# Optimization experiments

Measured on AMD Instinct MI355X. Metric: run time of the kernel, lower is better.

The kernel has to match this reference:

```python
import jax, jax.numpy as jnp
import numpy as np


def _lstm_selu(x, W, U, b):
    """Keras-semantics LSTM with activation='selu', return_sequences=True.
    x: [B, T, F]; W: [F, 4H]; U: [H, 4H]; b: [4H]. Gate order i, f, g, o.
    """
    B = x.shape[0]
    H = U.shape[0]
    # Precompute the input projection for all timesteps (one big GEMM).
    xz = jnp.einsum('btf,fg->btg', x, W) + b  # [B, T, 4H]

    def step(carry, xt):
        h, c = carry
        z = xt + h @ U  # [B, 4H]
        i, f, g, o = jnp.split(z, 4, axis=-1)
        i = jax.nn.sigmoid(i)
        f = jax.nn.sigmoid(f)
        g = jax.nn.selu(g)          # activation='selu' on candidate
        o = jax.nn.sigmoid(o)
        c = f * c + i * g
        h = o * jax.nn.selu(c)      # activation='selu' on cell output
        return (h, c), h

    h0 = jnp.zeros((B, H), x.dtype)
    c0 = jnp.zeros((B, H), x.dtype)
    (_, _), hs = jax.lax.scan(step, (h0, c0), jnp.swapaxes(xz, 0, 1))  # hs: [T, B, H]
    return jnp.swapaxes(hs, 0, 1)  # [B, T, H]


def setup_inputs() -> dict:
    key = jax.random.key(0)
    ks = jax.random.split(key, 6)
    B, T, F, H = 64, 2048, 64, 128
    s_in1 = 1.0 / np.sqrt(F)
    s_rec = 1.0 / np.sqrt(H)
    return {
        'x': jax.random.normal(ks[0], (B, T, F), dtype=jnp.float32),
        'W1': jax.random.normal(ks[1], (F, 4 * H), dtype=jnp.float32) * s_in1,
        'U1': jax.random.normal(ks[2], (H, 4 * H), dtype=jnp.float32) * s_rec,
        'b1': jnp.zeros((4 * H,), dtype=jnp.float32),
        'W2': jax.random.normal(ks[3], (H, 4 * H), dtype=jnp.float32) * s_rec,
        'U2': jax.random.normal(ks[4], (H, 4 * H), dtype=jnp.float32) * s_rec,
        'b2': jnp.zeros((4 * H,), dtype=jnp.float32),
    }


def reference(x, W1, U1, b1, W2, U2, b2):
    h1 = _lstm_selu(x, W1, U1, b1)   # layer 1, return_sequences=True
    h2 = _lstm_selu(h1, W2, U2, b2)  # layer 2 consumes layer-1 sequence
    return h2
```

## Files before the change

kernel.cpp:

```cpp
#include <hip/hip_runtime.h>
#include <hip/hip_bf16.h>

#define BATCH 64
#define SEQT  2048
#define FEAT  64
#define HID   128
#define G4    512
#define CHUNK 16
#define NCHUNK (SEQT / CHUNK)
#define XSP  68
#define H1P  136
#define XZP  516

using short8  = __attribute__((ext_vector_type(8))) short;
using floatx4 = __attribute__((ext_vector_type(4))) float;

#define BAR_LGKM() asm volatile("s_waitcnt lgkmcnt(0)\n\ts_barrier" ::: "memory")

__device__ __forceinline__ float sigmoidf_(float x) {
    return __builtin_amdgcn_rcpf(1.0f + __expf(-x));
}
__device__ __forceinline__ float seluf_(float x) {
    const float a = 1.6732632423543772f;
    const float s = 1.0507009873554805f;
    return x > 0.0f ? s * x : s * a * (__expf(x) - 1.0f);
}
__device__ __forceinline__ unsigned short f2bf_(float f) {
    unsigned u = __float_as_uint(f);
    u += 0x7FFFu + ((u >> 16) & 1u);
    return (unsigned short)(u >> 16);
}

__global__ __launch_bounds__(512)
__attribute__((amdgpu_waves_per_eu(2, 2)))
void fused_lstm(const float* __restrict__ x,
                const float* __restrict__ W1,
                const float* __restrict__ U1,
                const float* __restrict__ b1,
                const float* __restrict__ W2,
                const float* __restrict__ U2,
                const float* __restrict__ b2,
                unsigned long long* __restrict__ h1g,
                unsigned* __restrict__ flags,
                float* __restrict__ out) {
    const bool l2  = blockIdx.x >= BATCH;
    const int  b   = l2 ? ((int)blockIdx.x - BATCH) : (int)blockIdx.x;
    const int tid  = threadIdx.x;
    const int w    = tid >> 6;
    const int lane = tid & 63;
    const int c16  = lane & 15;
    const int quad = lane >> 4;
    const int j    = w * 16 + c16;

    __shared__ __align__(16) short hA[2][HID];
    __shared__ __align__(16) float xzbuf[CHUNK * XZP];
    __shared__ __align__(16) float xs[CHUNK * XSP];
    __shared__ __align__(16) short h1c[CHUNK * H1P];
    __shared__ __align__(16) short h1buf[CHUNK * HID];
    __shared__ __align__(16) float hbuf[CHUNK * HID];

    const float* U = l2 ? U2 : U1;
    short8 bfrag[4][4];
#pragma unroll
    for (int g = 0; g < 4; ++g) {
        const float* Ucol = U + (size_t)(g * 128 + j);
#pragma unroll
        for (int kc = 0; kc < 4; ++kc) {
            short8 v;
#pragma unroll
            for (int jj = 0; jj < 8; ++jj) {
                int k = kc * 32 + quad * 8 + jj;
                v[jj] = (short)f2bf_(Ucol[(size_t)k * G4]);
            }
            bfrag[g][kc] = v;
        }
    }

    const float* Wp = l2 ? W2 : W1;
    const int KCW = l2 ? 4 : 2;
    short8 wfrag[4][4];
#pragma unroll
    for (int g = 0; g < 4; ++g) {
        const float* Wcol = Wp + (size_t)(g * 128 + j);
#pragma unroll
        for (int kc = 0; kc < 4; ++kc) {
            if (kc < KCW) {
                short8 v;
#pragma unroll
                for (int jj = 0; jj < 8; ++jj) {
                    int k = kc * 32 + quad * 8 + jj;
                    v[jj] = (short)f2bf_(Wcol[(size_t)k * G4]);
                }
                wfrag[g][kc] = v;
            }
        }
    }
    const float* bb = l2 ? b2 : b1;
    const float4 bias4 = make_float4(bb[j], bb[128 + j], bb[256 + j], bb[384 + j]);

    const float* xb = x + (size_t)b * SEQT * FEAT;
    if (!l2) {
        if (tid < 256) {
            float4 v = ((const float4*)xb)[tid];
            *(float4*)&xs[(tid >> 4) * XSP + ((tid & 15) << 2)] = v;
        }
    }
    if (tid < HID) hA[0][tid] = 0;
    float cst = 0.0f;
    floatx4 zero4 = {0.f, 0.f, 0.f, 0.f};
    __syncthreads();

    float*              out_b = out + (size_t)b * SEQT * HID;
    unsigned long long* h1g_b = h1g + (size_t)b * (SEQT * HID / 4);

    for (int c = 0; c < NCHUNK; ++c) {
        float4 pf;
        if (!l2) {
            if (c + 1 < NCHUNK && tid < 256)
                pf = ((const float4*)(xb + (size_t)(c + 1) * CHUNK * FEAT))[tid];
            short8 ax[2];
#pragma unroll
            for (int kc = 0; kc < 2; ++kc) {
                const float* p = &xs[c16 * XSP + kc * 32 + quad * 8];
                float4 f0 = *(const float4*)p;
                float4 f1 = *(const float4*)(p + 4);
                short8 v;
                v[0] = (short)f2bf_(f0.x); v[1] = (short)f2bf_(f0.y);
                v[2] = (short)f2bf_(f0.z); v[3] = (short)f2bf_(f0.w);
                v[4] = (short)f2bf_(f1.x); v[5] = (short)f2bf_(f1.y);
                v[6] = (short)f2bf_(f1.z); v[7] = (short)f2bf_(f1.w);
                ax[kc] = v;
            }
            floatx4 acc1[4];
#pragma unroll
            for (int g = 0; g < 4; ++g) {
                floatx4 t = __builtin_amdgcn_mfma_f32_16x16x32_bf16(ax[0], wfrag[g][0], zero4, 0, 0, 0);
                acc1[g] = __builtin_amdgcn_mfma_f32_16x16x32_bf16(ax[1], wfrag[g][1], t, 0, 0, 0);
            }
#pragma unroll
            for (int r = 0; r < 4; ++r) {
                int srow = quad * 4 + r;
                *(float4*)&xzbuf[srow * XZP + j * 4] =
                    make_float4(acc1[0][r] + bias4.x, acc1[1][r] + bias4.y,
                                acc1[2][r] + bias4.z, acc1[3][r] + bias4.w);
            }
            __syncthreads();
        } else {
            if (tid == 0) {
                while (__hip_atomic_load(&flags[b], __ATOMIC_RELAXED,
                                         __HIP_MEMORY_SCOPE_AGENT) < (unsigned)(c + 1))
                    __builtin_amdgcn_s_sleep(2);
            }
            __syncthreads();
            {
                unsigned long long hv = __hip_atomic_load(
                    h1g_b + (size_t)c * 512 + tid, __ATOMIC_RELAXED, __HIP_MEMORY_SCOPE_AGENT);
                int t = tid >> 5, kg = tid & 31;
                *(unsigned long long*)&h1c[t * H1P + kg * 4] = hv;
            }
            __syncthreads();

            short8 ah[4];
#pragma unroll
            for (int kc = 0; kc < 4; ++kc)
                ah[kc] = *(const short8*)&h1c[c16 * H1P + kc * 32 + quad * 8];
            floatx4 acc2[4];
#pragma unroll
            for (int g = 0; g < 4; ++g) {
                floatx4 t = __builtin_amdgcn_mfma_f32_16x16x32_bf16(ah[0], wfrag[g][0], zero4, 0, 0, 0);
                t = __builtin_amdgcn_mfma_f32_16x16x32_bf16(ah[1], wfrag[g][1], t, 0, 0, 0);
                t = __builtin_amdgcn_mfma_f32_16x16x32_bf16(ah[2], wfrag[g][2], t, 0, 0, 0);
                acc2[g] = __builtin_amdgcn_mfma_f32_16x16x32_bf16(ah[3], wfrag[g][3], t, 0, 0, 0);
            }
#pragma unroll
            for (int r = 0; r < 4; ++r) {
                int srow = quad * 4 + r;
                *(float4*)&xzbuf[srow * XZP + j * 4] =
                    make_float4(acc2[0][r] + bias4.x, acc2[1][r] + bias4.y,
                                acc2[2][r] + bias4.z, acc2[3][r] + bias4.w);
            }
            __syncthreads();
        }

#pragma unroll 2
        for (int s = 0; s < CHUNK; ++s) {
            float4 xq = *(const float4*)&xzbuf[s * XZP + j * 4];
            const short* hb = &hA[s & 1][0];
            short8 af[4];
#pragma unroll
            for (int kc = 0; kc < 4; ++kc)
                af[kc] = *(const short8*)&hb[kc * 32 + quad * 8];

            floatx4 accA[4], accB[4];
#pragma unroll
            for (int g = 0; g < 4; ++g) {
                floatx4 t0 = __builtin_amdgcn_mfma_f32_16x16x32_bf16(af[0], bfrag[g][0], zero4, 0, 0, 0);
                accA[g] = __builtin_amdgcn_mfma_f32_16x16x32_bf16(af[1], bfrag[g][1], t0, 0, 0, 0);
                floatx4 t1 = __builtin_amdgcn_mfma_f32_16x16x32_bf16(af[2], bfrag[g][2], zero4, 0, 0, 0);
                accB[g] = __builtin_amdgcn_mfma_f32_16x16x32_bf16(af[3], bfrag[g][3], t1, 0, 0, 0);
            }

            float zi = accA[0][0] + accB[0][0] + xq.x;
            float zf = accA[1][0] + accB[1][0] + xq.y;
            float zg = accA[2][0] + accB[2][0] + xq.z;
            float zo = accA[3][0] + accB[3][0] + xq.w;
            float ig = sigmoidf_(zi), fg = sigmoidf_(zf);
            float gg = seluf_(zg),   og = sigmoidf_(zo);
            cst = fg * cst + ig * gg;
            float h = og * seluf_(cst);

            if (lane < 16) {
                unsigned short h16 = f2bf_(h);
                hA[(s + 1) & 1][j] = (short)h16;
                if (l2) hbuf[s * HID + j] = h;
                else    h1buf[s * HID + j] = (short)h16;
            }
            BAR_LGKM();
        }

        if (!l2) {
            unsigned long long hv = *(const unsigned long long*)&h1buf[tid * 4];
            __hip_atomic_store(h1g_b + (size_t)c * 512 + tid, hv,
                               __ATOMIC_RELAXED, __HIP_MEMORY_SCOPE_AGENT);
            if (c + 1 < NCHUNK && tid < 256)
                *(float4*)&xs[(tid >> 4) * XSP + ((tid & 15) << 2)] = pf;
            __syncthreads();
            if (tid == 0)
                __hip_atomic_store(&flags[b], (unsigned)(c + 1),
                                   __ATOMIC_RELAXED, __HIP_MEMORY_SCOPE_AGENT);
        } else {
            float4 hv = *(const float4*)&hbuf[tid * 4];
            *(float4*)&out_b[(size_t)c * CHUNK * HID + tid * 4] = hv;
        }
    }
}

extern "C" void kernel_launch(void* const* d_in, const int* in_sizes, int n_in,
                              void* d_out, int out_size, void* d_ws, size_t ws_size,
                              hipStream_t stream) {
    const float* x  = (const float*)d_in[0];
    const float* W1 = (const float*)d_in[1];
    const float* U1 = (const float*)d_in[2];
    const float* b1 = (const float*)d_in[3];
    const float* W2 = (const float*)d_in[4];
    const float* U2 = (const float*)d_in[5];
    const float* b2 = (const float*)d_in[6];
    float* out = (float*)d_out;

    const size_t BT       = (size_t)BATCH * SEQT;
    const size_t H1_BYTES = BT * HID * 2;

    unsigned long long* h1g   = (unsigned long long*)d_ws;
    unsigned*           flags = (unsigned*)((char*)d_ws + H1_BYTES);

    hipMemsetAsync(flags, 0, BATCH * sizeof(unsigned), stream);

    fused_lstm<<<dim3(2 * BATCH), dim3(512), 0, stream>>>(
        x, W1, U1, b1, W2, U2, b2, h1g, flags, out);
}
```

Before: 1.287 ms.

## Double chunk size to 32 and write layer-2 outputs directly to global

Raises the timestep chunk from 16 to 32, so the input-projection MFMAs, the flag polling, the cross-layer handoff and their block barriers run half as often, each covering two 16-row M tiles. Layer 2 now stores each h value straight to global memory inside the step loop rather than staging a chunk in shared memory and copying it out. The larger chunk increases the lag before layer 2 can start and raises shared-memory use. The per-step scattered global stores add traffic to the latency-critical recurrent loop.

```diff
diff --git a/kernel.cpp b/kernel.cpp
--- a/kernel.cpp
+++ b/kernel.cpp
@@ -6,7 +6,7 @@
 #define FEAT  64
 #define HID   128
 #define G4    512
-#define CHUNK 16
+#define CHUNK 32
 #define NCHUNK (SEQT / CHUNK)
 #define XSP  68
 #define H1P  136
@@ -57,7 +57,6 @@
     __shared__ __align__(16) float xs[CHUNK * XSP];
     __shared__ __align__(16) short h1c[CHUNK * H1P];
     __shared__ __align__(16) short h1buf[CHUNK * HID];
-    __shared__ __align__(16) float hbuf[CHUNK * HID];
 
     const float* U = l2 ? U2 : U1;
     short8 bfrag[4][4];
@@ -100,10 +99,8 @@
 
     const float* xb = x + (size_t)b * SEQT * FEAT;
     if (!l2) {
-        if (tid < 256) {
-            float4 v = ((const float4*)xb)[tid];
-            *(float4*)&xs[(tid >> 4) * XSP + ((tid & 15) << 2)] = v;
-        }
+        float4 v = ((const float4*)xb)[tid];
+        *(float4*)&xs[(tid >> 4) * XSP + ((tid & 15) << 2)] = v;
     }
     if (tid < HID) hA[0][tid] = 0;
     float cst = 0.0f;
@@ -116,33 +113,36 @@
     for (int c = 0; c < NCHUNK; ++c) {
         float4 pf;
         if (!l2) {
-            if (c + 1 < NCHUNK && tid < 256)
+            if (c + 1 < NCHUNK)
                 pf = ((const float4*)(xb + (size_t)(c + 1) * CHUNK * FEAT))[tid];
-            short8 ax[2];
-#pragma unroll
-            for (int kc = 0; kc < 2; ++kc) {
-                const float* p = &xs[c16 * XSP + kc * 32 + quad * 8];
-                float4 f0 = *(const float4*)p;
-                float4 f1 = *(const float4*)(p + 4);
-                short8 v;
-                v[0] = (short)f2bf_(f0.x); v[1] = (short)f2bf_(f0.y);
-                v[2] = (short)f2bf_(f0.z); v[3] = (short)f2bf_(f0.w);
-                v[4] = (short)f2bf_(f1.x); v[5] = (short)f2bf_(f1.y);
-                v[6] = (short)f2bf_(f1.z); v[7] = (short)f2bf_(f1.w);
-                ax[kc] = v;
-            }
-            floatx4 acc1[4];
-#pragma unroll
-            for (int g = 0; g < 4; ++g) {
-                floatx4 t = __builtin_amdgcn_mfma_f32_16x16x32_bf16(ax[0], wfrag[g][0], zero4, 0, 0, 0);
-                acc1[g] = __builtin_amdgcn_mfma_f32_16x16x32_bf16(ax[1], wfrag[g][1], t, 0, 0, 0);
-            }
-#pragma unroll
-            for (int r = 0; r < 4; ++r) {
-                int srow = quad * 4 + r;
-                *(float4*)&xzbuf[srow * XZP + j * 4] =
-                    make_float4(acc1[0][r] + bias4.x, acc1[1][r] + bias4.y,
-                                acc1[2][r] + bias4.z, acc1[3][r] + bias4.w);
+#pragma unroll
+            for (int mt = 0; mt < 2; ++mt) {
+                short8 ax[2];
+#pragma unroll
+                for (int kc = 0; kc < 2; ++kc) {
+                    const float* p = &xs[(mt * 16 + c16) * XSP + kc * 32 + quad * 8];
+                    float4 f0 = *(const float4*)p;
+                    float4 f1 = *(const float4*)(p + 4);
+                    short8 v;
+                    v[0] = (short)f2bf_(f0.x); v[1] = (short)f2bf_(f0.y);
+                    v[2] = (short)f2bf_(f0.z); v[3] = (short)f2bf_(f0.w);
+                    v[4] = (short)f2bf_(f1.x); v[5] = (short)f2bf_(f1.y);
+                    v[6] = (short)f2bf_(f1.z); v[7] = (short)f2bf_(f1.w);
+                    ax[kc] = v;
+                }
+                floatx4 acc1[4];
+#pragma unroll
+                for (int g = 0; g < 4; ++g) {
+                    floatx4 t = __builtin_amdgcn_mfma_f32_16x16x32_bf16(ax[0], wfrag[g][0], zero4, 0, 0, 0);
+                    acc1[g] = __builtin_amdgcn_mfma_f32_16x16x32_bf16(ax[1], wfrag[g][1], t, 0, 0, 0);
+                }
+#pragma unroll
+                for (int r = 0; r < 4; ++r) {
+                    int srow = mt * 16 + quad * 4 + r;
+                    *(float4*)&xzbuf[srow * XZP + j * 4] =
+                        make_float4(acc1[0][r] + bias4.x, acc1[1][r] + bias4.y,
+                                    acc1[2][r] + bias4.z, acc1[3][r] + bias4.w);
+                }
             }
             __syncthreads();
         } else {
@@ -152,32 +152,36 @@
                     __builtin_amdgcn_s_sleep(2);
             }
             __syncthreads();
-            {
+#pragma unroll
+            for (int i = 0; i < 2; ++i) {
+                int idx = tid + i * 512;
                 unsigned long long hv = __hip_atomic_load(
-                    h1g_b + (size_t)c * 512 + tid, __ATOMIC_RELAXED, __HIP_MEMORY_SCOPE_AGENT);
-                int t = tid >> 5, kg = tid & 31;
-                *(unsigned long long*)&h1c[t * H1P + kg * 4] = hv;
-            }
-            __syncthreads();
-
-            short8 ah[4];
-#pragma unroll
-            for (int kc = 0; kc < 4; ++kc)
-                ah[kc] = *(const short8*)&h1c[c16 * H1P + kc * 32 + quad * 8];
-            floatx4 acc2[4];
-#pragma unroll
-            for (int g = 0; g < 4; ++g) {
-                floatx4 t = __builtin_amdgcn_mfma_f32_16x16x32_bf16(ah[0], wfrag[g][0], zero4, 0, 0, 0);
-                t = __builtin_amdgcn_mfma_f32_16x16x32_bf16(ah[1], wfrag[g][1], t, 0, 0, 0);
-                t = __builtin_amdgcn_mfma_f32_16x16x32_bf16(ah[2], wfrag[g][2], t, 0, 0, 0);
-                acc2[g] = __builtin_amdgcn_mfma_f32_16x16x32_bf16(ah[3], wfrag[g][3], t, 0, 0, 0);
-            }
-#pragma unroll
-            for (int r = 0; r < 4; ++r) {
-                int srow = quad * 4 + r;
-                *(float4*)&xzbuf[srow * XZP + j * 4] =
-                    make_float4(acc2[0][r] + bias4.x, acc2[1][r] + bias4.y,
-                                acc2[2][r] + bias4.z, acc2[3][r] + bias4.w);
+                    h1g_b + (size_t)c * 1024 + idx, __ATOMIC_RELAXED, __HIP_MEMORY_SCOPE_AGENT);
+                *(unsigned long long*)&h1c[(idx >> 5) * H1P + (idx & 31) * 4] = hv;
+            }
+            __syncthreads();
+
+#pragma unroll
+            for (int mt = 0; mt < 2; ++mt) {
+                short8 ah[4];
+#pragma unroll
+                for (int kc = 0; kc < 4; ++kc)
+                    ah[kc] = *(const short8*)&h1c[(mt * 16 + c16) * H1P + kc * 32 + quad * 8];
+                floatx4 acc2[4];
+#pragma unroll
+                for (int g = 0; g < 4; ++g) {
+                    floatx4 t = __builtin_amdgcn_mfma_f32_16x16x32_bf16(ah[0], wfrag[g][0], zero4, 0, 0, 0);
+                    t = __builtin_amdgcn_mfma_f32_16x16x32_bf16(ah[1], wfrag[g][1], t, 0, 0, 0);
+                    t = __builtin_amdgcn_mfma_f32_16x16x32_bf16(ah[2], wfrag[g][2], t, 0, 0, 0);
+                    acc2[g] = __builtin_amdgcn_mfma_f32_16x16x32_bf16(ah[3], wfrag[g][3], t, 0, 0, 0);
+                }
+#pragma unroll
+                for (int r = 0; r < 4; ++r) {
+                    int srow = mt * 16 + quad * 4 + r;
+                    *(float4*)&xzbuf[srow * XZP + j * 4] =
+                        make_float4(acc2[0][r] + bias4.x, acc2[1][r] + bias4.y,
+                                    acc2[2][r] + bias4.z, acc2[3][r] + bias4.w);
+                }
             }
             __syncthreads();
         }
@@ -212,25 +216,26 @@
             if (lane < 16) {
                 unsigned short h16 = f2bf_(h);
                 hA[(s + 1) & 1][j] = (short)h16;
-                if (l2) hbuf[s * HID + j] = h;
+                if (l2) out_b[(size_t)(c * CHUNK + s) * HID + j] = h;
                 else    h1buf[s * HID + j] = (short)h16;
             }
             BAR_LGKM();
         }
 
         if (!l2) {
-            unsigned long long hv = *(const unsigned long long*)&h1buf[tid * 4];
-            __hip_atomic_store(h1g_b + (size_t)c * 512 + tid, hv,
-                               __ATOMIC_RELAXED, __HIP_MEMORY_SCOPE_AGENT);
-            if (c + 1 < NCHUNK && tid < 256)
+#pragma unroll
+            for (int i = 0; i < 2; ++i) {
+                int idx = tid + i * 512;
+                unsigned long long hv = *(const unsigned long long*)&h1buf[idx * 4];
+                __hip_atomic_store(h1g_b + (size_t)c * 1024 + idx, hv,
+                                   __ATOMIC_RELAXED, __HIP_MEMORY_SCOPE_AGENT);
+            }
+            if (c + 1 < NCHUNK)
                 *(float4*)&xs[(tid >> 4) * XSP + ((tid & 15) << 2)] = pf;
             __syncthreads();
             if (tid == 0)
                 __hip_atomic_store(&flags[b], (unsigned)(c + 1),
                                    __ATOMIC_RELAXED, __HIP_MEMORY_SCOPE_AGENT);
-        } else {
-            float4 hv = *(const float4*)&hbuf[tid * 4];
-            *(float4*)&out_b[(size_t)c * CHUNK * HID + tid * 4] = hv;
         }
     }
 }
```

Result: faster. 1.259 ms (-2.2%).
